# Optimization experiments

Hardware: AMD Instinct MI355X
Metric: run time of the kernel (lower is better)

Reference implementation:

```python
import jax, jax.numpy as jnp
import numpy as np

EPS = 1e-12
S = 1          # support_num
K_NB = 50      # neighbor_num
CLASS_NUM = 50
CAT_NUM = 16


def _normalize(x, axis):
    n = jnp.sqrt(jnp.sum(x * x, axis=axis, keepdims=True))
    return x / jnp.maximum(n, EPS)


def _knn(v, k):
    # v: (b, n, 3) -> (b, n, k) indices of k nearest neighbors (self excluded)
    sq = jnp.sum(v * v, axis=-1)
    d2 = sq[:, :, None] + sq[:, None, :] - 2.0 * jnp.einsum('bnd,bmd->bnm', v, v)
    _, idx = jax.lax.top_k(-d2, k + 1)
    return idx[:, :, 1:]


def _gather(t, idx):
    # t: (b, v, c), idx: (b, v1, k) -> (b, v1, k, c)
    b = t.shape[0]
    return t[jnp.arange(b)[:, None, None], idx]


def _nb_dir(v, idx):
    nb = _gather(v, idx)                        # (b, v, k, 3)
    return _normalize(nb - v[:, :, None, :], -1)


def _bn(x, g, b):
    # x: (b, n, c); BatchNorm1d in training mode: batch stats over (b, n)
    m = jnp.mean(x, axis=(0, 1))
    va = jnp.var(x, axis=(0, 1))
    return (x - m) * jax.lax.rsqrt(va + 1e-5) * g + b


def _conv_surface(idx, v, directions, kernel_num):
    dirs = _normalize(directions, 0)            # (3, S*kernel_num)
    theta = jax.nn.relu(jnp.einsum('bvnd,dm->bvnm', _nb_dir(v, idx), dirs))
    b, vn, k, _ = theta.shape
    theta = theta.reshape(b, vn, k, S, kernel_num)
    return jnp.sum(jnp.max(theta, axis=2), axis=2)     # (b, v, kernel_num)


def _conv_layer(idx, v, fm, w, bias, directions, out_ch):
    dirs = _normalize(directions, 0)            # (3, S*out_ch)
    theta = jax.nn.relu(jnp.einsum('bvnd,dm->bvnm', _nb_dir(v, idx), dirs))
    fout = fm @ w + bias                        # (b, v, (S+1)*out_ch)
    fc = fout[..., :out_ch]
    fs = _gather(fout[..., out_ch:], idx)       # (b, v, k, S*out_ch)
    b, vn, k = idx.shape
    act = (theta * fs).reshape(b, vn, k, S, out_ch)
    return fc + jnp.sum(jnp.max(act, axis=2), axis=2)


def _pool(v, fm, rate, nb):
    idx = _knn(v, nb)
    pooled = jnp.max(_gather(fm, idx), axis=2)
    pn = v.shape[1] // rate
    # original uses randperm; deterministic subsample of first pn points here
    return v[:, :pn], pooled[:, :pn]


def _sa(x, qk, vw, vb, tw, tb, g, be):
    # PCT-style offset-attention; x: (b, n, c); q and k share weights
    q = jnp.einsum('bnc,qc->bnq', x, qk)
    k = jnp.einsum('bnc,qc->bnq', x, qk)
    v = jnp.einsum('bnc,oc->bno', x, vw) + vb
    attn = jax.nn.softmax(jnp.einsum('bnq,bmq->bnm', q, k), axis=-1)
    attn = attn / (1e-9 + jnp.sum(attn, axis=1, keepdims=True))
    x_r = jnp.einsum('bno,bnm->bmo', v, attn)
    pre = jnp.einsum('bno,co->bnc', x - x_r, tw) + tb
    return x + jax.nn.relu(_bn(pre, g, be))


def _nearest(target, source):
    d2 = (jnp.sum(target * target, -1)[:, :, None]
          + jnp.sum(source * source, -1)[:, None, :]
          - 2.0 * jnp.einsum('bnd,bmd->bnm', target, source))
    return jnp.argmin(d2, axis=-1)              # (b, n)


def _up(fm, idx):
    b = fm.shape[0]
    return fm[jnp.arange(b)[:, None], idx]


def setup_inputs() -> dict:
    key = jax.random.key(0)
    cnt = [0]
    def nk():
        cnt[0] += 1
        return jax.random.fold_in(key, cnt[0])
    def rn(shape, scale=0.05):
        return jax.random.normal(nk(), shape, dtype=jnp.float32) * scale
    d = {}
    d['vertices'] = jax.random.normal(nk(), (8, 3, 2048), dtype=jnp.float32)
    d['onehot'] = jax.random.uniform(nk(), (8, CAT_NUM), dtype=jnp.float32)
    def sa(pfx, c):
        d[pfx + '_qk'] = rn((c // 4, c)); d[pfx + '_vw'] = rn((c, c))
        d[pfx + '_vb'] = jnp.zeros((c,), jnp.float32)
        d[pfx + '_tw'] = rn((c, c)); d[pfx + '_tb'] = jnp.zeros((c,), jnp.float32)
        d[pfx + '_g'] = jnp.ones((c,), jnp.float32); d[pfx + '_be'] = jnp.zeros((c,), jnp.float32)
    def conv(pfx, cin, cout):
        d[pfx + '_w'] = rn((cin, (S + 1) * cout)); d[pfx + '_b'] = rn(((S + 1) * cout,))
        d[pfx + '_dir'] = rn((3, S * cout))
    def bn(pfx, c):
        d[pfx + '_g'] = jnp.ones((c,), jnp.float32); d[pfx + '_b'] = jnp.zeros((c,), jnp.float32)
    d['conv0_dir'] = rn((3, S * 128)); bn('bn0', 128); sa('sa0', 128)
    conv('conv1', 128, 128); bn('bn1', 128); sa('sa1', 128)
    conv('conv2', 128, 256); bn('bn2', 256); sa('sa2', 256)
    conv('conv3', 256, 256); bn('bn3', 256); sa('sa3', 256)
    conv('conv4', 256, 512); sa('sa4', 512)
    dim_fuse = 128 + 128 + 256 + 256 + 512 + 512 + CAT_NUM   # 1808
    d['h1_w'] = rn((dim_fuse, 512)); d['h1_b'] = jnp.zeros((512,), jnp.float32)
    d['h2_w'] = rn((512, 512)); d['h2_b'] = jnp.zeros((512,), jnp.float32)
    d['h3_w'] = rn((512, CLASS_NUM)); d['h3_b'] = jnp.zeros((CLASS_NUM,), jnp.float32)
    return d


def reference(vertices, onehot, conv0_dir, bn0_g, bn0_b,
              sa0_qk, sa0_vw, sa0_vb, sa0_tw, sa0_tb, sa0_g, sa0_be,
              conv1_w, conv1_b, conv1_dir, bn1_g, bn1_b,
              sa1_qk, sa1_vw, sa1_vb, sa1_tw, sa1_tb, sa1_g, sa1_be,
              conv2_w, conv2_b, conv2_dir, bn2_g, bn2_b,
              sa2_qk, sa2_vw, sa2_vb, sa2_tw, sa2_tb, sa2_g, sa2_be,
              conv3_w, conv3_b, conv3_dir, bn3_g, bn3_b,
              sa3_qk, sa3_vw, sa3_vb, sa3_tw, sa3_tb, sa3_g, sa3_be,
              conv4_w, conv4_b, conv4_dir,
              sa4_qk, sa4_vw, sa4_vb, sa4_tw, sa4_tb, sa4_g, sa4_be,
              h1_w, h1_b, h2_w, h2_b, h3_w, h3_b):
    v = jnp.transpose(vertices, (0, 2, 1))      # (b, n, 3)
    bs, n, _ = v.shape
    idx = _knn(v, K_NB)
    fm0 = jax.nn.relu(_bn(_conv_surface(idx, v, conv0_dir, 128), bn0_g, bn0_b))
    fm0 = _sa(fm0, sa0_qk, sa0_vw, sa0_vb, sa0_tw, sa0_tb, sa0_g, sa0_be)
    fm1 = jax.nn.relu(_bn(_conv_layer(idx, v, fm0, conv1_w, conv1_b, conv1_dir, 128), bn1_g, bn1_b))
    fm1 = _sa(fm1, sa1_qk, sa1_vw, sa1_vb, sa1_tw, sa1_tb, sa1_g, sa1_be)
    v1, fmp1 = _pool(v, fm1, 4, 4)              # (b, n/4, .)
    idx1 = _knn(v1, K_NB)
    fm2 = jax.nn.relu(_bn(_conv_layer(idx1, v1, fmp1, conv2_w, conv2_b, conv2_dir, 256), bn2_g, bn2_b))
    fm2 = _sa(fm2, sa2_qk, sa2_vw, sa2_vb, sa2_tw, sa2_tb, sa2_g, sa2_be)
    fm3 = jax.nn.relu(_bn(_conv_layer(idx1, v1, fm2, conv3_w, conv3_b, conv3_dir, 256), bn3_g, bn3_b))
    fm3 = _sa(fm3, sa3_qk, sa3_vw, sa3_vb, sa3_tw, sa3_tb, sa3_g, sa3_be)
    v2, fmp2 = _pool(v1, fm3, 4, 4)             # (b, n/16, .)
    idx2 = _knn(v2, K_NB)
    fm4 = _conv_layer(idx2, v2, fmp2, conv4_w, conv4_b, conv4_dir, 512)
    fm4 = _sa(fm4, sa4_qk, sa4_vw, sa4_vb, sa4_tw, sa4_tb, sa4_g, sa4_be)
    f_glob = jnp.max(fm4, axis=1)               # (b, 512)
    ni1 = _nearest(v, v1)
    ni2 = _nearest(v, v2)
    fm2u = _up(fm2, ni1)
    fm3u = _up(fm3, ni1)
    fm4u = _up(fm4, ni2)
    fuse = jnp.concatenate([
        fm0, fm1, fm2u, fm3u, fm4u,
        jnp.broadcast_to(f_glob[:, None, :], (bs, n, f_glob.shape[-1])),
        jnp.broadcast_to(onehot[:, None, :], (bs, n, onehot.shape[-1])),
    ], axis=2)                                  # (b, n, 1808)
    x = jax.nn.relu(fuse @ h1_w + h1_b)
    x = jax.nn.relu(x @ h2_w + h2_b)
    logits = x @ h3_w + h3_b
    return jax.nn.log_softmax(logits, axis=-1)  # (b, n, class_num)
```

## Files before the change

kernel.cpp:

```cpp
#include <hip/hip_runtime.h>
#include <cfloat>


#define BB   8
#define NP0  2048
#define NP1  512
#define NP2  128
#define KNB_ 50
#define VS0  (NP0 * 3)

typedef __attribute__((ext_vector_type(8))) short short8_t;
typedef __attribute__((ext_vector_type(4))) short short4_t;
typedef __attribute__((ext_vector_type(4))) float f32x4_t;
typedef unsigned short u16;

static constexpr size_t O_V0    = 0;
static constexpr size_t O_IDX0  = 196608;
static constexpr size_t O_IDXP0 = 3473408;
static constexpr size_t O_IDX1  = 3538944;
static constexpr size_t O_IDXP1 = 4358144;
static constexpr size_t O_IDX2  = 4374528;
static constexpr size_t O_NI1   = 4579328;
static constexpr size_t O_NI2   = 4644864;
static constexpr size_t O_FGLOB = 4710400;
// ... 155 lines not shown
      if constexpr (OUTM == 0) {
        float* Cp = (float*)C1 + (size_t)z * sC;
#pragma unroll
        for (int q = 0; q < 4; ++q) {
          float vv = acc[i][j][q] + bv;
          if (ACC) vv += Cp[(size_t)(gr0 + q) * N + gc];
          Cp[(size_t)(gr0 + q) * N + gc] = vv;
        }
      } else if constexpr (OUTM == 1) {
        u16* Ph = (u16*)C1 + (size_t)z * sC;
        u16* Pl = (u16*)C2 + (size_t)z * sC;
#pragma unroll
        for (int q = 0; q < 4; ++q) {
          float vv = acc[i][j][q] + bv;
          u16 h = f2bf(vv);
          Ph[(size_t)(gr0 + q) * N + gc] = h;
          Pl[(size_t)(gr0 + q) * N + gc] = f2bf(vv - bf2f(h));
        }
      } else if constexpr (OUTM == 2) {
        u16* Ph = (u16*)C1 + (size_t)z * sC;
        u16* Pl = (u16*)C2 + (size_t)z * sC;
        short4_t h4, l4;
#pragma unroll
        for (int q = 0; q < 4; ++q) {
          float vv = acc[i][j][q] + bv;
          u16 h = f2bf(vv);
          h4[q] = (short)h;
          l4[q] = (short)f2bf(vv - bf2f(h));
        }
        *(short4_t*)(Ph + (size_t)gc * M + gr0) = h4;
        *(short4_t*)(Pl + (size_t)gc * M + gr0) = l4;
      } else if constexpr (OUTM == 4) {
        if (gc < QQ) {
          u16* Ph = (u16*)C1 + (size_t)zb * sC;
          u16* Pl = (u16*)C2 + (size_t)zb * sC;
#pragma unroll
          for (int q = 0; q < 4; ++q) {
            float vv = acc[i][j][q];
            u16 h = f2bf(vv);
            Ph[(size_t)(gr0 + q) * QQ + gc] = h;
            Pl[(size_t)(gr0 + q) * QQ + gc] = f2bf(vv - bf2f(h));
          }
        } else {
          const int cv = gc - QQ;
          const float bv2 = bias[cv];
          u16* Th = (u16*)C3 + (size_t)zb * sCv;
          u16* Tl = (u16*)C4 + (size_t)zb * sCv;
          short4_t h4, l4;
#pragma unroll
          for (int q = 0; q < 4; ++q) {
            float vv = acc[i][j][q] + bv2;
            u16 h = f2bf(vv);
            h4[q] = (short)h;
            l4[q] = (short)f2bf(vv - bf2f(h));
          }
          *(short4_t*)(Th + (size_t)cv * M + gr0) = h4;
          *(short4_t*)(Tl + (size_t)cv * M + gr0) = l4;
        }
      } else {
        u16* Cb = (u16*)C1 + (size_t)z * sC;
#pragma unroll
        for (int q = 0; q < 4; ++q) {
          float vv = fmaxf(acc[i][j][q] + bv, 0.f);
          Cb[(size_t)(gr0 + q) * N + gc] = f2bf(vv);
        }
      }
    }
  }
}

template <int TM, int AMODE, int BIASM, int OUTM, bool ACC, bool GIDX, bool BSPLIT = true>
static void mmp(hipStream_t st, const void* A1, const void* A2,
                const u16* Bh, const u16* Bl, const float* bias,
                void* C1, void* C2, int M, int N, int K,
                long sA, long sB, long sC, int Z, int ksplit,
                const int* gidx = nullptr, long sG = 0,
                void* C3 = nullptr, void* C4 = nullptr, int QQ = 0, long sCv = 0) {
  dim3 grid(M / TM, (N + TM - 1) / TM, Z * ksplit);
  k_mmp<TM, AMODE, BIASM, OUTM, ACC, GIDX, BSPLIT><<<grid, 256, 0, st>>>(
      A1, A2, Bh, Bl, bias, C1, C2, M, N, K, sA, sB, sC, ksplit, gidx, sG,
      C3, C4, QQ, sCv);
}

template <int QD>
__global__ __launch_bounds__(256) void k_sa_stats(
    const u16* __restrict__ qh, const u16* __restrict__ ql, int N,
    float* __restrict__ mx, float* __restrict__ inv) {
  __shared__ float mr[2][64], sr[2][64];
  const int b = blockIdx.y;
  const int m0 = blockIdx.x * 64;
  const int t = threadIdx.x, lane = t & 63, w = t >> 6;
  const int wm = (w >> 1) * 32, wn = (w & 1) * 64;
  const int frow = lane & 15, kq = (lane >> 4) * 8;
  const u16* qhb = qh + (size_t)b * N * QD;
  const u16* qlb = ql + (size_t)b * N * QD;
  constexpr int KS = QD / 32;
  short8_t ahq[KS][2], alq[KS][2];
#pragma unroll
  for (int ks = 0; ks < KS; ++ks)
#pragma unroll
    for (int i = 0; i < 2; ++i) {
      const size_t r = (size_t)(m0 + wm + i * 16 + frow) * QD + ks * 32 + kq;
      ahq[ks][i] = *(const short8_t*)(qhb + r);
      alq[ks][i] = *(const short8_t*)(qlb + r);
    }
  float M[2][4], S[2][4];
#pragma unroll
  for (int i = 0; i < 2; ++i)
#pragma unroll
    for (int q = 0; q < 4; ++q) { M[i][q] = -FLT_MAX; S[i][q] = 0.f; }

  for (int n0 = 0; n0 < N; n0 += 128) {
    f32x4_t acc[2][4];
#pragma unroll
    for (int i = 0; i < 2; ++i)
#pragma unroll
      for (int j = 0; j < 4; ++j) acc[i][j] = (f32x4_t){0.f, 0.f, 0.f, 0.f};
#pragma unroll
    for (int ks = 0; ks < KS; ++ks) {
      short8_t b_h[4], b_l[4];
#pragma unroll
      for (int j = 0; j < 4; ++j) {
        const size_t r = (size_t)(n0 + wn + j * 16 + frow) * QD + ks * 32 + kq;
        b_h[j] = *(const short8_t*)(qhb + r);
        b_l[j] = *(const short8_t*)(qlb + r);
      }
#pragma unroll
      for (int i = 0; i < 2; ++i)
#pragma unroll
        for (int j = 0; j < 4; ++j) {
          acc[i][j] = __builtin_amdgcn_mfma_f32_16x16x32_bf16(ahq[ks][i], b_h[j], acc[i][j], 0, 0, 0);
          acc[i][j] = __builtin_amdgcn_mfma_f32_16x16x32_bf16(ahq[ks][i], b_l[j], acc[i][j], 0, 0, 0);
          acc[i][j] = __builtin_amdgcn_mfma_f32_16x16x32_bf16(alq[ks][i], b_h[j], acc[i][j], 0, 0, 0);
        }
    }
#pragma unroll
    for (int i = 0; i < 2; ++i)
#pragma unroll
      for (int q = 0; q < 4; ++q) {
        float tm = acc[i][0][q];
#pragma unroll
        for (int j = 1; j < 4; ++j) tm = fmaxf(tm, acc[i][j][q]);
#pragma unroll
        for (int off = 1; off < 16; off <<= 1) tm = fmaxf(tm, __shfl_xor(tm, off));
        const float Mn = fmaxf(M[i][q], tm);
        float ps = 0.f;
#pragma unroll
        for (int j = 0; j < 4; ++j) ps += __expf(acc[i][j][q] - Mn);
#pragma unroll
        for (int off = 1; off < 16; off <<= 1) ps += __shfl_xor(ps, off);
        S[i][q] = S[i][q] * __expf(M[i][q] - Mn) + ps;
        M[i][q] = Mn;
      }
  }
  if (frow == 0) {
#pragma unroll
    for (int i = 0; i < 2; ++i)
#pragma unroll
      for (int q = 0; q < 4; ++q) {
        const int ml = wm + i * 16 + (lane >> 4) * 4 + q;
        mr[w & 1][ml] = M[i][q];
        sr[w & 1][ml] = S[i][q];
      }
  }
  __syncthreads();
  if (t < 64) {
    const float M0 = mr[0][t], M1 = mr[1][t];
    const float Mm = fmaxf(M0, M1);
    const float Sm = sr[0][t] * __expf(M0 - Mm) + sr[1][t] * __expf(M1 - Mm);
    mx[(size_t)b * N + m0 + t] = Mm;
    inv[(size_t)b * N + m0 + t] = 1.f / Sm;
  }
}

template <int QD, int NSPLIT>
__global__ __launch_bounds__(256) void k_sa_xr(
    const u16* __restrict__ qh, const u16* __restrict__ ql,
    const u16* __restrict__ vmh, const u16* __restrict__ vml,
    const float* __restrict__ mx, const float* __restrict__ inv,
    const float* __restrict__ xcur, u16* __restrict__ xsh, u16* __restrict__ xsl,
    float* __restrict__ xrp, float* __restrict__ csump,
    int N, int C) {
  __shared__ __align__(16) u16 Ph[64][132];
  __shared__ __align__(16) u16 Vh[128][68], Vl[128][68];
  const int b = blockIdx.z / NSPLIT, sidx = blockIdx.z % NSPLIT;
  const int m0 = blockIdx.x * 64, c0 = blockIdx.y * 128;
  const int t = threadIdx.x, lane = t & 63, w = t >> 6;
  const int wm = (w >> 1) * 32, wn = (w & 1) * 64;
  const int frow = lane & 15, kq = (lane >> 4) * 8;
  const u16* qhb = qh + (size_t)b * N * QD;
  const u16* qlb = ql + (size_t)b * N * QD;
  const u16* vhb = vmh + (size_t)b * (size_t)N * C;
  const u16* vlb = vml + (size_t)b * (size_t)N * C;
  const float* mxb = mx + (size_t)b * N;
  const float* invb = inv + (size_t)b * N;
  constexpr int KS = QD / 32;
  const int vr = t >> 1, vco = (t & 1) * 32;
  short8_t ahq[KS][2], alq[KS][2];
#pragma unroll
  for (int ks = 0; ks < KS; ++ks)
#pragma unroll
    for (int i = 0; i < 2; ++i) {
      const size_t r = (size_t)(m0 + wm + i * 16 + frow) * QD + ks * 32 + kq;
      ahq[ks][i] = *(const short8_t*)(qhb + r);
      alq[ks][i] = *(const short8_t*)(qlb + r);
    }
  f32x4_t xacc[2][4];
  float csum[2][4];
#pragma unroll
  for (int i = 0; i < 2; ++i)
#pragma unroll
    for (int j = 0; j < 4; ++j) { xacc[i][j] = (f32x4_t){0.f, 0.f, 0.f, 0.f}; csum[i][j] = 0.f; }

  const int nlo = sidx * (N / NSPLIT), nhi = nlo + N / NSPLIT;
  for (int n0 = nlo; n0 < nhi; n0 += 128) {
    __syncthreads();
    {
      const u16* s1 = vhb + (size_t)(c0 + vr) * N + n0 + vco;
      const u16* s2 = vlb + (size_t)(c0 + vr) * N + n0 + vco;
#pragma unroll
      for (int u = 0; u < 4; ++u) {
        *(short8_t*)&Vh[vr][vco + u * 8] = *(const short8_t*)(s1 + u * 8);
        *(short8_t*)&Vl[vr][vco + u * 8] = *(const short8_t*)(s2 + u * 8);
      }
    }
    f32x4_t acc[2][4];
#pragma unroll
    for (int i = 0; i < 2; ++i)
#pragma unroll
      for (int j = 0; j < 4; ++j) acc[i][j] = (f32x4_t){0.f, 0.f, 0.f, 0.f};
#pragma unroll
    for (int ks = 0; ks < KS; ++ks) {
      short8_t b_h[4], b_l[4];
#pragma unroll
      for (int j = 0; j < 4; ++j) {
        const size_t r = (size_t)(n0 + wn + j * 16 + frow) * QD + ks * 32 + kq;
        b_h[j] = *(const short8_t*)(qhb + r);
        b_l[j] = *(const short8_t*)(qlb + r);
      }
#pragma unroll
      for (int i = 0; i < 2; ++i)
#pragma unroll
        for (int j = 0; j < 4; ++j) {
          acc[i][j] = __builtin_amdgcn_mfma_f32_16x16x32_bf16(ahq[ks][i], b_h[j], acc[i][j], 0, 0, 0);
          acc[i][j] = __builtin_amdgcn_mfma_f32_16x16x32_bf16(ahq[ks][i], b_l[j], acc[i][j], 0, 0, 0);
          acc[i][j] = __builtin_amdgcn_mfma_f32_16x16x32_bf16(alq[ks][i], b_h[j], acc[i][j], 0, 0, 0);
        }
    }
    float mxj[4], ivj[4];
#pragma unroll
    for (int j = 0; j < 4; ++j) {
      const int n = n0 + wn + j * 16 + frow;
      mxj[j] = mxb[n];
      ivj[j] = invb[n];
    }
// ... 142 lines not shown
    else v = jb.s[i];
    u16 h = f2bf(v);
    jb.dh[i] = h;
    jb.dl[i] = f2bf(v - bf2f(h));
  }
}

template <bool RELU, bool LO>
__global__ void k_split4(const float* __restrict__ x, u16* __restrict__ ph,
                         u16* __restrict__ pl, int n4) {
  int i = blockIdx.x * 256 + threadIdx.x;
  if (i >= n4) return;
  float4 v = ((const float4*)x)[i];
  short4_t h4, l4;
  float vv[4] = {v.x, v.y, v.z, v.w};
#pragma unroll
  for (int q = 0; q < 4; ++q) {
    float f = RELU ? fmaxf(vv[q], 0.f) : vv[q];
    u16 h = f2bf(f);
    h4[q] = (short)h;
    if (LO) l4[q] = (short)f2bf(f - bf2f(h));
  }
  *(short4_t*)(ph + (size_t)i * 4) = h4;
  if (LO) *(short4_t*)(pl + (size_t)i * 4) = l4;
}

__global__ void k_xcat(const u16* __restrict__ f0, const u16* __restrict__ f1,
                       const u16* __restrict__ f2, const u16* __restrict__ f3,
                       const u16* __restrict__ f4, const int* __restrict__ ni1,
                       const int* __restrict__ ni2, u16* __restrict__ xcat, int b0) {
  const int G = 1280 / 8;
  int i = blockIdx.x * 256 + threadIdx.x;
  if (i >= 4 * NP0 * G) return;
  const int g = i % G, n = (i / G) % NP0, bl = i / (G * NP0);
  const int b = b0 + bl;
  const int k = g * 8;
  short8_t v;
  if (k < 128)      v = *(const short8_t*)(f0 + ((size_t)b * NP0 + n) * 128 + k);
  else if (k < 256) v = *(const short8_t*)(f1 + ((size_t)b * NP0 + n) * 128 + (k - 128));
  else if (k < 512) v = *(const short8_t*)(f2 + ((size_t)b * NP1 + ni1[b * NP0 + n]) * 256 + (k - 256));
  else if (k < 768) v = *(const short8_t*)(f3 + ((size_t)b * NP1 + ni1[b * NP0 + n]) * 256 + (k - 512));
  else              v = *(const short8_t*)(f4 + ((size_t)b * NP2 + ni2[b * NP0 + n]) * 512 + (k - 768));
  *(short8_t*)(xcat + ((size_t)bl * NP0 + n) * 1280 + k) = v;
}

template <int NCAND, int KSEL>
__global__ __launch_bounds__(256) void k_knn_radix(const float4* __restrict__ v4,
                                                   int Nq, int* __restrict__ outIdx) {
  const int b = blockIdx.y;
  const int wave = threadIdx.x >> 6, lane = threadIdx.x & 63;
  const int qi = blockIdx.x * 4 + wave;
  const float4* vb4 = v4 + (size_t)b * NP0;
  const float4 qp = vb4[qi];
  constexpr int CH = NCAND / 64;
  unsigned d[CH];
  unsigned x[32];
#pragma unroll
  for (int j = 0; j < 32; ++j) x[j] = 0u;
#pragma unroll
  for (int j = 0; j < CH; ++j) {
    const int m = lane + j * 64;
    const float4 cp = vb4[m];
    const float dx = cp.x - qp.x, dy = cp.y - qp.y, dz = cp.z - qp.z;
    const float dd = dx * dx + dy * dy + dz * dz;
    d[j] = __float_as_uint((m == qi) ? FLT_MAX : dd);
    x[j] = d[j];
  }
#pragma unroll
  for (int st = 0; st < 5; ++st) {
    const int s = 16 >> st;
    const unsigned ml = (s == 16) ? 0x0000FFFFu : (s == 8) ? 0x00FF00FFu
                      : (s == 4) ? 0x0F0F0F0Fu : (s == 2) ? 0x33333333u : 0x55555555u;
#pragma unroll
    for (int i = 0; i < 32; ++i) {
      if (i & s) continue;
      unsigned t = ((x[i] >> s) ^ x[i + s]) & ml;
      x[i + s] ^= t;
      x[i] ^= (t << s);
    }
  }
  unsigned active = (CH == 32) ? 0xFFFFFFFFu : ((1u << CH) - 1u);
  unsigned T = 0u;
  int kk = KSEL;
#pragma unroll
  for (int bb = 30; bb >= 2; bb -= 2) {
    const unsigned mh = x[bb], mlo = x[bb - 1];
    const unsigned a00 = active & ~mh & ~mlo;
    const unsigned a01 = active & ~mh & mlo;
    const unsigned a10 = active & mh & ~mlo;
    unsigned pA = (unsigned)__popc(a00) | ((unsigned)__popc(a01) << 16);
    unsigned pB = (unsigned)__popc(a10);
#pragma unroll
    for (int off = 32; off; off >>= 1) {
      pA += __shfl_xor(pA, off);
      pB += __shfl_xor(pB, off);
    }
    const int C00 = (int)(pA & 0xFFFFu), C01 = (int)(pA >> 16), C10 = (int)pB;
    if (kk <= C00) {
      active = a00;
    } else if (kk <= C00 + C01) {
      kk -= C00; active = a01; T |= 1u << (bb - 1);
    } else if (kk <= C00 + C01 + C10) {
      kk -= C00 + C01; active = a10; T |= 1u << bb;
    } else {
      kk -= C00 + C01 + C10; active = active & mh & mlo; T |= 3u << (bb - 1);
    }
  }
  {
    const unsigned zn = active & ~x[0];
    int c0 = __popc(zn);
#pragma unroll
    for (int off = 32; off; off >>= 1) c0 += __shfl_xor(c0, off);
    if (kk <= c0) active = zn;
    else { active &= x[0]; T |= 1u; }
  }
  int* orow = outIdx + ((size_t)b * Nq + qi) * KSEL;
  const unsigned long long ltmask = (1ull << lane) - 1ull;
  int base = 0;
#pragma unroll
  for (int j = 0; j < CH; ++j) {
    const bool sel = d[j] < T;
    const unsigned long long bal = __ballot(sel);
    const int pos = base + (int)__popcll(bal & ltmask);
    if (sel) orow[pos] = lane + j * 64;
    base += (int)__popcll(bal);
  }
  for (int j = 0; j < CH; ++j) {
    if (base >= KSEL) break;
    const bool sel = ((active >> j) & 1u) != 0u;
    const unsigned long long bal = __ballot(sel);
    const int pos = base + (int)__popcll(bal & ltmask);
    if (sel && pos < KSEL) orow[pos] = lane + j * 64;
    base += (int)__popcll(bal);
  }
}

template <int NCAND, int KSEL>
__global__ __launch_bounds__(256) void k_knn2(const float4* __restrict__ v4,
                                              int Nq, int* __restrict__ outIdx) {
  const int b = blockIdx.y;
  const int wave = threadIdx.x >> 6, lane = threadIdx.x & 63;
  const int qi = blockIdx.x * 4 + wave;
  const float4* vb4 = v4 + (size_t)b * NP0;
  const float4 qp = vb4[qi];
  constexpr int CH = NCAND / 64;
  float d[CH];
#pragma unroll
  for (int j = 0; j < CH; ++j) {
    const int m = lane + j * 64;
    const float4 cp = vb4[m];
    const float dx = cp.x - qp.x, dy = cp.y - qp.y, dz = cp.z - qp.z;
    const float dd = dx * dx + dy * dy + dz * dz;
    d[j] = (m == qi) ? FLT_MAX : dd;
  }
  int* orow = outIdx + ((size_t)b * Nq + qi) * KSEL;
#pragma unroll 1
  for (int s = 0; s < KSEL; ++s) {
    float bd = FLT_MAX; int bj = 0;
#pragma unroll
    for (int j = 0; j < CH; ++j) {
      const bool better = d[j] < bd;
      bd = better ? d[j] : bd;
      bj = better ? j : bj;
    }
    int bm = lane + bj * 64;
#pragma unroll
    for (int off = 32; off; off >>= 1) {
      const float od = __shfl_xor(bd, off);
      const int om = __shfl_xor(bm, off);
      if (od < bd || (od == bd && om < bm)) { bd = od; bm = om; }
    }
    if (lane == 0) orow[s] = bm;
#pragma unroll
    for (int j = 0; j < CH; ++j)
      if (bm == lane + j * 64) d[j] = FLT_MAX;
  }
}

__global__ void k_transpose(const float* __restrict__ in, float* __restrict__ out,
                            float* __restrict__ out4) {
  int i = blockIdx.x * 256 + threadIdx.x;
  if (i >= BB * NP0 * 3) return;
  int dd = i % 3, tt = (i / 3) % NP0, b = i / (3 * NP0);
  float v = in[((size_t)b * 3 + dd) * NP0 + tt];
  out[i] = v;
  out4[((size_t)b * NP0 + tt) * 4 + dd] = v;
}

__global__ void k_conv_surface(const float* __restrict__ v, const int* __restrict__ idx,
                               const float* __restrict__ dirs, float* __restrict__ out,
                               int N, int M) {
// ... 101 lines not shown
  v = fmaxf(v, 0.f);
  float r = ADD ? base[i] + v : v;
  outf[i] = r;
  u16 h = f2bf(r);
  ph[i] = h;
  pl[i] = f2bf(r - bf2f(h));
}

__global__ void k_pool(const u16* __restrict__ fh, const u16* __restrict__ fl,
                       const int* __restrict__ idxp, u16* __restrict__ oh,
                       u16* __restrict__ ol, int Nin, int pn, int C) {
  int b = blockIdx.y, p = blockIdx.x, c = threadIdx.x;
  const int* ir = idxp + ((size_t)b * pn + p) * 4;
  const u16* fhb = fh + (size_t)b * Nin * C;
  const u16* flb = fl + (size_t)b * Nin * C;
  float acc = -FLT_MAX;
#pragma unroll
  for (int k = 0; k < 4; ++k) {
    size_t o = (size_t)ir[k] * C + c;
    acc = fmaxf(acc, bf2f(fhb[o]) + bf2f(flb[o]));
  }
  u16 h = f2bf(acc);
  oh[((size_t)b * pn + p) * C + c] = h;
  ol[((size_t)b * pn + p) * C + c] = f2bf(acc - bf2f(h));
}

__global__ void k_maxn(const u16* __restrict__ fh, const u16* __restrict__ fl,
                       float* __restrict__ out, int N, int C) {
  int b = blockIdx.y;
  int c = blockIdx.x * 256 + threadIdx.x;
  if (c >= C) return;
  float acc = -FLT_MAX;
  for (int n = 0; n < N; ++n) {
    size_t o = ((size_t)b * N + n) * C + c;
    acc = fmaxf(acc, bf2f(fh[o]) + bf2f(fl[o]));
  }
  out[(size_t)b * C + c] = acc;
}

__global__ void k_nearest(const float* __restrict__ v, int Ns, int* __restrict__ out) {
  extern __shared__ float sp[];
  int b = blockIdx.y;
  const float* vsb = v + (size_t)b * VS0;
  for (int i = threadIdx.x; i < Ns * 3; i += 256) sp[i] = vsb[i];
  __syncthreads();
  int t = blockIdx.x * 256 + threadIdx.x;
  float tx = vsb[t * 3], ty = vsb[t * 3 + 1], tz = vsb[t * 3 + 2];
  float bd = FLT_MAX; int bi = 0;
#pragma unroll 4
  for (int s = 0; s < Ns; ++s) {
    float dx = sp[s * 3] - tx, dy = sp[s * 3 + 1] - ty, dz = sp[s * 3 + 2] - tz;
    float dd = dx * dx + dy * dy + dz * dz;
    if (dd < bd) { bd = dd; bi = s; }
  }
  out[(size_t)b * NP0 + t] = bi;
}

__global__ void k_glob1(const float* __restrict__ fglob, const float* __restrict__ onehot,
                        const float* __restrict__ h1w, const float* __restrict__ h1b,
                        float* __restrict__ out) {
  int b = blockIdx.x, j = threadIdx.x;
  float s = h1b[j];
  for (int i = 0; i < 512; ++i) s = fmaf(fglob[b * 512 + i], h1w[(size_t)(1280 + i) * 512 + j], s);
  for (int i = 0; i < 16; ++i) s = fmaf(onehot[b * 16 + i], h1w[(size_t)(1792 + i) * 512 + j], s);
  out[b * 512 + j] = s;
}

__global__ void k_logsoftmax(float* __restrict__ x, int rows, int C) {
  int r = blockIdx.x * 4 + (threadIdx.x >> 6);
  int lane = threadIdx.x & 63;
  if (r >= rows) return;
  float* xr = x + (size_t)r * C;
  float v = (lane < C) ? xr[lane] : -FLT_MAX;
  float mx = v;
  for (int o = 32; o; o >>= 1) mx = fmaxf(mx, __shfl_xor(mx, o));
  float e = (lane < C) ? __expf(v - mx) : 0.f;
  float s = e;
  for (int o = 32; o; o >>= 1) s += __shfl_xor(s, o);
  float lse = mx + logf(s);
  if (lane < C) xr[lane] = v - lse;
}

struct Ws {
  float *v0, *v4, *fglob, *glob1, *mx, *inv, *csump, *stats, *bpart, *xcur, *pre, *fout, *xrp;
  int *idx0, *idxp0, *idx1, *idxp1, *idx2, *ni1, *ni2;
  u16 *wh, *wl;
  u16 *fm0h, *fm0l, *fm1h, *fm1l, *fm2h, *fm2l, *fm3h, *fm3l, *fm4h, *fm4l;
  u16 *fmp1h, *fmp1l, *fmp2h, *fmp2l, *qh, *ql, *vmh, *vml, *xsh, *xsl;
  u16 *x1h, *x2b, *xcat;
};

static void run_sa(hipStream_t st, Ws& ws, int N, int C, int Q,
                   const u16* qkvh, const u16* qkvl, const u16* twh, const u16* twl,
                   const float* vb, const float* tb, const float* g, const float* be,
                   u16* xh, u16* xl) {
  const long sx = (long)N * C;
  mmp<64, 0, 0, 4, false, false>(st, xh, xl, qkvh, qkvl, vb, ws.qh, ws.ql,
                                 N, Q + C, C, sx, 0, (long)N * Q, BB, 1,
                                 nullptr, 0, ws.vmh, ws.vml, Q, sx);
  dim3 gs(N / 64, BB);
  if (Q == 32) {
    k_sa_stats<32><<<gs, 256, 0, st>>>(ws.qh, ws.ql, N, ws.mx, ws.inv);
    dim3 gx(N / 64, C / 128, BB * 2);
    k_sa_xr<32, 2><<<gx, 256, 0, st>>>(ws.qh, ws.ql, ws.vmh, ws.vml, ws.mx, ws.inv,
                                       nullptr, nullptr, nullptr, ws.xrp, ws.csump, N, C);
    k_xsub2<2><<<((size_t)BB * N * C + 255) / 256, 256, 0, st>>>(
        ws.xrp, ws.csump, ws.xcur, ws.xsh, ws.xsl, N, C);
  } else if (Q == 64) {
    k_sa_stats<64><<<gs, 256, 0, st>>>(ws.qh, ws.ql, N, ws.mx, ws.inv);
    dim3 gx(N / 64, C / 128, BB * 4);
    k_sa_xr<64, 4><<<gx, 256, 0, st>>>(ws.qh, ws.ql, ws.vmh, ws.vml, ws.mx, ws.inv,
                                       nullptr, nullptr, nullptr, ws.xrp, ws.csump, N, C);
    k_xsub2<4><<<((size_t)BB * N * C + 255) / 256, 256, 0, st>>>(
        ws.xrp, ws.csump, ws.xcur, ws.xsh, ws.xsl, N, C);
  } else {
    k_sa_stats<128><<<gs, 256, 0, st>>>(ws.qh, ws.ql, N, ws.mx, ws.inv);
    dim3 gx(N / 64, C / 128, BB);
    k_sa_xr<128, 1><<<gx, 256, 0, st>>>(ws.qh, ws.ql, ws.vmh, ws.vml, ws.mx, ws.inv,
                                        ws.xcur, ws.xsh, ws.xsl, nullptr, nullptr, N, C);
  }
  mmp<64, 0, 1, 0, false, false>(st, ws.xsh, ws.xsl, twh, twl, tb, ws.pre, nullptr,
                                 N, C, C, sx, 0, sx, BB, 1);
  k_bn_part<<<256, 256, 0, st>>>(ws.pre, BB * N, C, ws.bpart);
  k_bn_fin<<<(C + 31) / 32, 256, 0, st>>>(ws.bpart, BB * N, C, ws.stats);
  k_bn_apply<true><<<(BB * N * C + 255) / 256, 256, 0, st>>>(ws.pre, ws.stats, g, be,
                                                             ws.xcur, ws.xcur, xh, xl, BB * N * C, C);
}

static void run_conv(hipStream_t st, Ws& ws, const u16* finh, const u16* finl, int Cin,
                     const u16* cwh, const u16* cwl, const float* bias, const float* dirs,
                     const int* idx, int N, int C,
                     const float* bng, const float* bnb, bool doBN, u16* fmh, u16* fml) {
  if (N == NP0)
    mmp<128, 0, 1, 0, false, false>(st, finh, finl, cwh, cwl, bias, ws.fout, nullptr,
                                    N, 2 * C, Cin, (long)N * Cin, 0, (long)N * 2 * C, BB, 1);
  else
    mmp<64, 0, 1, 0, false, false>(st, finh, finl, cwh, cwl, bias, ws.fout, nullptr,
                                   N, 2 * C, Cin, (long)N * Cin, 0, (long)N * 2 * C, BB, 1);
  k_conv_layer<<<dim3(N, BB), C, 0, st>>>(ws.v0, idx, dirs, ws.fout, ws.xcur, N, C);
  if (doBN) {
    k_bn_part<<<256, 256, 0, st>>>(ws.xcur, BB * N, C, ws.bpart);
    k_bn_fin<<<(C + 31) / 32, 256, 0, st>>>(ws.bpart, BB * N, C, ws.stats);
    k_bn_apply<false><<<(BB * N * C + 255) / 256, 256, 0, st>>>(
        ws.xcur, ws.stats, bng, bnb, nullptr, ws.xcur, fmh, fml, BB * N * C, C);
  } else {
    k_split4<false, true><<<(BB * N * C / 4 + 255) / 256, 256, 0, st>>>(
        ws.xcur, fmh, fml, BB * N * C / 4);
  }
}

extern "C" void kernel_launch(void* const* d_in, const int* in_sizes, int n_in,
                              void* d_out, int out_size, void* d_ws, size_t ws_size,
                              hipStream_t stream) {
  auto in = [&](int i) { return (const float*)d_in[i]; };
  char* p = (char*)d_ws;
  Ws ws;
  ws.v0 = (float*)(p + O_V0);
  ws.v4 = (float*)(p + O_V4);
  ws.idx0 = (int*)(p + O_IDX0); ws.idxp0 = (int*)(p + O_IDXP0);
  ws.idx1 = (int*)(p + O_IDX1); ws.idxp1 = (int*)(p + O_IDXP1);
  ws.idx2 = (int*)(p + O_IDX2);
  ws.ni1 = (int*)(p + O_NI1); ws.ni2 = (int*)(p + O_NI2);
  ws.fglob = (float*)(p + O_FGLOB); ws.glob1 = (float*)(p + O_GLOB1);
  ws.mx = (float*)(p + O_COLS); ws.inv = (float*)(p + O_CPART);
  ws.csump = (float*)(p + O_CPART + 65536);
  ws.stats = (float*)(p + O_STATS); ws.bpart = (float*)(p + O_BPART);
  ws.xcur = (float*)(p + O_XCUR);
  ws.pre = (float*)(p + O_AREA);
  ws.fout = (float*)(p + O_AREA);
  ws.xrp = (float*)(p + O_AREA);
  ws.xcat = (u16*)(p + O_AREA);
  char* pl = p + O_PL;
  ws.wh = (u16*)(pl + PL_WH); ws.wl = (u16*)(pl + PL_WL);
  ws.fm0h = (u16*)(pl + PL_FM0H); ws.fm0l = (u16*)(pl + PL_FM0L);
  ws.fm1h = (u16*)(pl + PL_FM1H); ws.fm1l = (u16*)(pl + PL_FM1L);
  ws.fm2h = (u16*)(pl + PL_FM2H); ws.fm2l = (u16*)(pl + PL_FM2L);
  ws.fm3h = (u16*)(pl + PL_FM3H); ws.fm3l = (u16*)(pl + PL_FM3L);
  ws.fm4h = (u16*)(pl + PL_FM4H); ws.fm4l = (u16*)(pl + PL_FM4L);
  ws.fmp1h = (u16*)(pl + PL_FMP1H); ws.fmp1l = (u16*)(pl + PL_FMP1L);
  ws.fmp2h = (u16*)(pl + PL_FMP2H); ws.fmp2l = (u16*)(pl + PL_FMP2L);
  ws.qh = (u16*)(pl + PL_QH); ws.ql = (u16*)(pl + PL_QL);
  ws.vmh = (u16*)(pl + PL_VMH); ws.vml = (u16*)(pl + PL_VML);
  ws.xsh = (u16*)(pl + PL_XSH); ws.xsl = (u16*)(pl + PL_XSL);
  ws.x1h = (u16*)(pl + PL_X1H);
  ws.x2b = (u16*)(p + O_XCUR);
  float* out = (float*)d_out;

  SplitJobs jobs;
  size_t wq[22];
  size_t off = 0;
  int ji = 0;
  auto addjob = [&](const float* s, int K, int N, int trans) {
    int n = K * N;
    jobs.j[ji] = {s, ws.wh + off, ws.wl + off, n, K, N, trans};
    wq[ji] = off; off += (size_t)n; ++ji;
  };
  addjob(in(5), 128, 32, 0);  addjob(in(6), 128, 128, 0);  addjob(in(8), 128, 128, 0);
  addjob(in(17), 128, 32, 0); addjob(in(18), 128, 128, 0); addjob(in(20), 128, 128, 0);
  addjob(in(29), 256, 64, 0); addjob(in(30), 256, 256, 0); addjob(in(32), 256, 256, 0);
  addjob(in(41), 256, 64, 0); addjob(in(42), 256, 256, 0); addjob(in(44), 256, 256, 0);
  addjob(in(51), 512, 128, 0); addjob(in(52), 512, 512, 0); addjob(in(54), 512, 512, 0);
  addjob(in(12), 128, 256, 1);
  addjob(in(24), 128, 512, 1);
  addjob(in(36), 256, 512, 1);
  addjob(in(48), 256, 1024, 1);
  addjob(in(58), 1280, 512, 1);
  addjob(in(60), 512, 512, 1);
  addjob(in(62), 512, 50, 1);
  k_splitjobs<<<dim3(32, 22), 256, 0, stream>>>(jobs);
  auto W = [&](int i) { return ws.wh + wq[i]; };
  auto Wl = [&](int i) { return ws.wl + wq[i]; };

  k_transpose<<<(BB * NP0 * 3 + 255) / 256, 256, 0, stream>>>(in(0), ws.v0, ws.v4);
  k_knn_radix<NP0, KNB_><<<dim3(NP0 / 4, BB), 256, 0, stream>>>(
      (const float4*)ws.v4, NP0, ws.idx0);

  k_conv_surface<<<dim3(NP0, BB), 128, 0, stream>>>(ws.v0, ws.idx0, in(2), ws.xcur, NP0, 128);
  k_bn_part<<<256, 256, 0, stream>>>(ws.xcur, BB * NP0, 128, ws.bpart);
  k_bn_fin<<<4, 256, 0, stream>>>(ws.bpart, BB * NP0, 128, ws.stats);
  k_bn_apply<false><<<(BB * NP0 * 128 + 255) / 256, 256, 0, stream>>>(
      ws.xcur, ws.stats, in(3), in(4), nullptr, ws.xcur, ws.fm0h, ws.fm0l, BB * NP0 * 128, 128);

  run_sa(stream, ws, NP0, 128, 32, W(0), Wl(0), W(2), Wl(2),
         in(7), in(9), in(10), in(11), ws.fm0h, ws.fm0l);
  run_conv(stream, ws, ws.fm0h, ws.fm0l, 128, W(15), Wl(15), in(13), in(14), ws.idx0,
           NP0, 128, in(15), in(16), true, ws.fm1h, ws.fm1l);
  run_sa(stream, ws, NP0, 128, 32, W(3), Wl(3), W(5), Wl(5),
         in(19), in(21), in(22), in(23), ws.fm1h, ws.fm1l);

  k_knn2<NP0, 4><<<dim3(NP1 / 4, BB), 256, 0, stream>>>((const float4*)ws.v4, NP1, ws.idxp0);
  k_pool<<<dim3(NP1, BB), 128, 0, stream>>>(ws.fm1h, ws.fm1l, ws.idxp0,
                                            ws.fmp1h, ws.fmp1l, NP0, NP1, 128);
  k_knn_radix<NP1, KNB_><<<dim3(NP1 / 4, BB), 256, 0, stream>>>(
      (const float4*)ws.v4, NP1, ws.idx1);

  run_conv(stream, ws, ws.fmp1h, ws.fmp1l, 128, W(16), Wl(16), in(25), in(26), ws.idx1,
           NP1, 256, in(27), in(28), true, ws.fm2h, ws.fm2l);
  run_sa(stream, ws, NP1, 256, 64, W(6), Wl(6), W(8), Wl(8),
         in(31), in(33), in(34), in(35), ws.fm2h, ws.fm2l);
  run_conv(stream, ws, ws.fm2h, ws.fm2l, 256, W(17), Wl(17), in(37), in(38), ws.idx1,
           NP1, 256, in(39), in(40), true, ws.fm3h, ws.fm3l);
  run_sa(stream, ws, NP1, 256, 64, W(9), Wl(9), W(11), Wl(11),
         in(43), in(45), in(46), in(47), ws.fm3h, ws.fm3l);

  k_knn2<NP1, 4><<<dim3(NP2 / 4, BB), 256, 0, stream>>>((const float4*)ws.v4, NP2, ws.idxp1);
  k_pool<<<dim3(NP2, BB), 256, 0, stream>>>(ws.fm3h, ws.fm3l, ws.idxp1,
                                            ws.fmp2h, ws.fmp2l, NP1, NP2, 256);
  k_knn_radix<NP2, KNB_><<<dim3(NP2 / 4, BB), 256, 0, stream>>>(
      (const float4*)ws.v4, NP2, ws.idx2);
  run_conv(stream, ws, ws.fmp2h, ws.fmp2l, 256, W(18), Wl(18), in(49), in(50), ws.idx2,
           NP2, 512, nullptr, nullptr, false, ws.fm4h, ws.fm4l);
  run_sa(stream, ws, NP2, 512, 128, W(12), Wl(12), W(14), Wl(14),
         in(53), in(55), in(56), in(57), ws.fm4h, ws.fm4l);
// ... 23 lines not shown
```

Baseline: 1.273 ms.

## Split softmax stats over key range with merge kernel; early-exit radix top-k select

The attention softmax statistics kernel now splits the key dimension into 4 chunks across a third grid axis for Q=32/64 and writes partial max/sum values. A new merge kernel combines them using the log-sum-exp rescale. This adds parallelism for small grids (N=512/128 blocks per batch). Separately, the radix-select loop in the kNN top-k now tracks the active count and breaks early once the remaining candidates exactly fill k, and it is no longer unrolled. The split adds a kernel launch and a scratch buffer placed in a shared area, which must not alias live data.

Measured after the change: 1.181 ms. -7.2%, faster.

```diff
diff --git a/kernel.cpp b/kernel.cpp
--- a/kernel.cpp
+++ b/kernel.cpp
@@ -261,13 +261,15 @@
       C3, C4, QQ, sCv);
 }
 
-template <int QD>
+template <int QD, int NS>
 __global__ __launch_bounds__(256) void k_sa_stats(
     const u16* __restrict__ qh, const u16* __restrict__ ql, int N,
-    float* __restrict__ mx, float* __restrict__ inv) {
+    float* __restrict__ mx, float* __restrict__ inv,
+    float* __restrict__ Mp, float* __restrict__ Sp) {
   __shared__ float mr[2][64], sr[2][64];
   const int b = blockIdx.y;
   const int m0 = blockIdx.x * 64;
+  const int sidx = blockIdx.z;
   const int t = threadIdx.x, lane = t & 63, w = t >> 6;
   const int wm = (w >> 1) * 32, wn = (w & 1) * 64;
   const int frow = lane & 15, kq = (lane >> 4) * 8;
@@ -289,7 +291,8 @@
 #pragma unroll
     for (int q = 0; q < 4; ++q) { M[i][q] = -FLT_MAX; S[i][q] = 0.f; }
 
-  for (int n0 = 0; n0 < N; n0 += 128) {
+  const int nlo = sidx * (N / NS), nhi = nlo + N / NS;
+  for (int n0 = nlo; n0 < nhi; n0 += 128) {
     f32x4_t acc[2][4];
 #pragma unroll
     for (int i = 0; i < 2; ++i)
@@ -347,9 +350,31 @@
     const float M0 = mr[0][t], M1 = mr[1][t];
     const float Mm = fmaxf(M0, M1);
     const float Sm = sr[0][t] * __expf(M0 - Mm) + sr[1][t] * __expf(M1 - Mm);
-    mx[(size_t)b * N + m0 + t] = Mm;
-    inv[(size_t)b * N + m0 + t] = 1.f / Sm;
-  }
+    if constexpr (NS == 1) {
+      mx[(size_t)b * N + m0 + t] = Mm;
+      inv[(size_t)b * N + m0 + t] = 1.f / Sm;
+    } else {
+      const size_t o = ((size_t)sidx * BB + b) * N + m0 + t;
+      Mp[o] = Mm;
+      Sp[o] = Sm;
+    }
+  }
+}
+
+template <int NS>
+__global__ void k_smerge(const float* __restrict__ Mp, const float* __restrict__ Sp,
+                         float* __restrict__ mx, float* __restrict__ inv, int total) {
+  int i = blockIdx.x * 256 + threadIdx.x;
+  if (i >= total) return;
+  float M = -FLT_MAX;
+#pragma unroll
+  for (int s = 0; s < NS; ++s) M = fmaxf(M, Mp[(size_t)s * total + i]);
+  float S = 0.f;
+#pragma unroll
+  for (int s = 0; s < NS; ++s)
+    S += Sp[(size_t)s * total + i] * __expf(Mp[(size_t)s * total + i] - M);
+  mx[i] = M;
+  inv[i] = 1.f / S;
 }
 
 template <int QD, int NSPLIT>
@@ -658,7 +683,9 @@
   unsigned active = (CH == 32) ? 0xFFFFFFFFu : ((1u << CH) - 1u);
   unsigned T = 0u;
   int kk = KSEL;
-#pragma unroll
+  int actcnt = NCAND;
+  bool done = false;
+#pragma unroll 1
   for (int bb = 30; bb >= 2; bb -= 2) {
     const unsigned mh = x[bb], mlo = x[bb - 1];
     const unsigned a00 = active & ~mh & ~mlo;
@@ -673,16 +700,20 @@
     }
     const int C00 = (int)(pA & 0xFFFFu), C01 = (int)(pA >> 16), C10 = (int)pB;
     if (kk <= C00) {
-      active = a00;
+      active = a00; actcnt = C00;
     } else if (kk <= C00 + C01) {
-      kk -= C00; active = a01; T |= 1u << (bb - 1);
+      kk -= C00; active = a01; actcnt = C01; T |= 1u << (bb - 1);
     } else if (kk <= C00 + C01 + C10) {
-      kk -= C00 + C01; active = a10; T |= 1u << bb;
+      kk -= C00 + C01; active = a10; actcnt = C10; T |= 1u << bb;
     } else {
-      kk -= C00 + C01 + C10; active = active & mh & mlo; T |= 3u << (bb - 1);
-    }
-  }
-  {
+      kk -= C00 + C01 + C10;
+      active = active & mh & mlo;
+      actcnt = actcnt - C00 - C01 - C10;
+      T |= 3u << (bb - 1);
+    }
+    if (actcnt == kk) { done = true; break; }
+  }
+  if (!done) {
     const unsigned zn = active & ~x[0];
     int c0 = __popc(zn);
 #pragma unroll
@@ -950,7 +981,7 @@
 }
 
 struct Ws {
-  float *v0, *v4, *fglob, *glob1, *mx, *inv, *csump, *stats, *bpart, *xcur, *pre, *fout, *xrp;
+  float *v0, *v4, *fglob, *glob1, *mx, *inv, *csump, *stats, *bpart, *xcur, *pre, *fout, *xrp, *spart;
   int *idx0, *idxp0, *idx1, *idxp1, *idx2, *ni1, *ni2;
   u16 *wh, *wl;
   u16 *fm0h, *fm0l, *fm1h, *fm1l, *fm2h, *fm2l, *fm3h, *fm3l, *fm4h, *fm4l;
@@ -966,23 +997,29 @@
   mmp<64, 0, 0, 4, false, false>(st, xh, xl, qkvh, qkvl, vb, ws.qh, ws.ql,
                                  N, Q + C, C, sx, 0, (long)N * Q, BB, 1,
                                  nullptr, 0, ws.vmh, ws.vml, Q, sx);
-  dim3 gs(N / 64, BB);
   if (Q == 32) {
-    k_sa_stats<32><<<gs, 256, 0, st>>>(ws.qh, ws.ql, N, ws.mx, ws.inv);
+    float* Sp = ws.spart + (size_t)4 * BB * N;
+    k_sa_stats<32, 4><<<dim3(N / 64, BB, 4), 256, 0, st>>>(ws.qh, ws.ql, N,
+        nullptr, nullptr, ws.spart, Sp);
+    k_smerge<4><<<(BB * N + 255) / 256, 256, 0, st>>>(ws.spart, Sp, ws.mx, ws.inv, BB * N);
     dim3 gx(N / 64, C / 128, BB * 2);
     k_sa_xr<32, 2><<<gx, 256, 0, st>>>(ws.qh, ws.ql, ws.vmh, ws.vml, ws.mx, ws.inv,
                                        nullptr, nullptr, nullptr, ws.xrp, ws.csump, N, C);
     k_xsub2<2><<<((size_t)BB * N * C + 255) / 256, 256, 0, st>>>(
         ws.xrp, ws.csump, ws.xcur, ws.xsh, ws.xsl, N, C);
   } else if (Q == 64) {
-    k_sa_stats<64><<<gs, 256, 0, st>>>(ws.qh, ws.ql, N, ws.mx, ws.inv);
+    float* Sp = ws.spart + (size_t)4 * BB * N;
+    k_sa_stats<64, 4><<<dim3(N / 64, BB, 4), 256, 0, st>>>(ws.qh, ws.ql, N,
+        nullptr, nullptr, ws.spart, Sp);
+    k_smerge<4><<<(BB * N + 255) / 256, 256, 0, st>>>(ws.spart, Sp, ws.mx, ws.inv, BB * N);
     dim3 gx(N / 64, C / 128, BB * 4);
     k_sa_xr<64, 4><<<gx, 256, 0, st>>>(ws.qh, ws.ql, ws.vmh, ws.vml, ws.mx, ws.inv,
                                        nullptr, nullptr, nullptr, ws.xrp, ws.csump, N, C);
     k_xsub2<4><<<((size_t)BB * N * C + 255) / 256, 256, 0, st>>>(
         ws.xrp, ws.csump, ws.xcur, ws.xsh, ws.xsl, N, C);
   } else {
-    k_sa_stats<128><<<gs, 256, 0, st>>>(ws.qh, ws.ql, N, ws.mx, ws.inv);
+    k_sa_stats<128, 1><<<dim3(N / 64, BB, 1), 256, 0, st>>>(ws.qh, ws.ql, N,
+        ws.mx, ws.inv, nullptr, nullptr);
     dim3 gx(N / 64, C / 128, BB);
     k_sa_xr<128, 1><<<gx, 256, 0, st>>>(ws.qh, ws.ql, ws.vmh, ws.vml, ws.mx, ws.inv,
                                         ws.xcur, ws.xsh, ws.xsl, nullptr, nullptr, N, C);
@@ -1037,6 +1074,7 @@
   ws.pre = (float*)(p + O_AREA);
   ws.fout = (float*)(p + O_AREA);
   ws.xrp = (float*)(p + O_AREA);
+  ws.spart = (float*)(p + O_AREA);
   ws.xcat = (u16*)(p + O_AREA);
   char* pl = p + O_PL;
   ws.wh = (u16*)(pl + PL_WH); ws.wl = (u16*)(pl + PL_WL);
```
